# Kernel tuning notes

Measured on AMD Instinct MI355X. Metric: run time of the kernel, lower is better.

## Reference

```python
import jax, jax.numpy as jnp
import numpy as np

N_NODES = 50000
N_EDGES = 625000
D = 128          # hidden_dim
H = 8            # num_heads
DH = D // H      # head_dim
L = 4            # num_layers
F_IN = 64        # in_channels
G = 64           # num graphs
BETA = 1.0
EPS = 1e-5       # layernorm eps


def _seg_softmax(s, idx, n):
    # softmax of s over segments defined by idx (segments present in idx are never empty)
    m = jax.ops.segment_max(s, idx, num_segments=n)
    e = jnp.exp(s - m[idx])
    d = jax.ops.segment_sum(e, idx, num_segments=n)
    return e / d[idx]


def _ln(x, s, b):
    mu = jnp.mean(x, axis=-1, keepdims=True)
    var = jnp.var(x, axis=-1, keepdims=True)
    return (x - mu) / jnp.sqrt(var + EPS) * s + b


def _forward(x, edge_index, batch, node_W, node_b, cW1, cb1, cW2, cb2,
             qW, qb, kW, kb, vW, vb, oW, ob, bW, bb,
             f1W, f1b, f2W, f2b, n1s, n1b, n2s, n2b,
             outW1, outb1, outW2, outb2):
    N = x.shape[0]
    src, tgt = edge_index[0], edge_index[1]
    h = x @ node_W + node_b                              # [N, D]
    for l in range(L):
        # ---- dynamic curvature (attention-approximated Wasserstein) ----
        h_src, h_tgt = h[src], h[tgt]                    # [E, D]
        sim = jnp.sum(h_src * h_tgt, axis=-1) * BETA     # [E]
        alpha = _seg_softmax(sim, tgt, N)                # segment softmax over tgt
        dist = jnp.linalg.norm(h_src - h_tgt, axis=-1)   # [E]
        agg = jax.ops.segment_sum(alpha * dist, tgt, num_segments=N)
        curv = 1.0 - agg[tgt] / jnp.maximum(dist, 1e-6)  # [E]
        ce = jax.nn.relu(curv[:, None] @ cW1 + cb1) @ cW2 + cb2  # [E, D]
        # ---- CurvphormerLayer ----
        xn = _ln(h, n1s[l], n1b[l])
        q = (xn @ qW[l] + qb[l]).reshape(N, H, DH)
        k = (xn @ kW[l] + kb[l]).reshape(N, H, DH)
        v = (xn @ vW[l] + vb[l]).reshape(N, H, DH)
        scores = jnp.sum(q[src] * k[tgt], axis=-1) / (DH ** 0.5)  # [E, H]
        scores = scores + ce @ bW[l] + bb[l]                       # curvature bias
        probs = _seg_softmax(scores, tgt, N)                       # [E, H]
        msgs = (probs[..., None] * v[tgt]).reshape(-1, D)          # [E, D]
        aggm = jax.ops.segment_sum(msgs, src, num_segments=N)     # scatter to src
        h = h + (aggm @ oW[l] + ob[l])
        xn2 = _ln(h, n2s[l], n2b[l])
        h = h + (jax.nn.relu(xn2 @ f1W[l] + f1b[l]) @ f2W[l] + f2b[l])
    # ---- mean pool per graph ----
    counts = jnp.maximum(jax.ops.segment_sum(jnp.ones((N,), h.dtype), batch, num_segments=G), 1.0)
    g = jax.ops.segment_sum(h, batch, num_segments=G) / counts[:, None]
    return jax.nn.relu(g @ outW1 + outb1) @ outW2 + outb2


def setup_inputs() -> dict:
    keys = iter(jax.random.split(jax.random.key(0), 32))
    p = lambda shape, s=0.02: jax.random.normal(next(keys), shape, jnp.float32) * s
    x = jax.random.normal(next(keys), (N_NODES, F_IN), jnp.float32)
    edge_index = jax.random.randint(next(keys), (2, N_EDGES), 0, N_NODES)
    batch = jnp.sort(jax.random.randint(next(keys), (N_NODES,), 0, G))
    inp = {
        "x": x, "edge_index": edge_index, "batch": batch,
        "node_W": p((F_IN, D)), "node_b": p((D,)),
        "cW1": p((1, D)), "cb1": p((D,)), "cW2": p((D, D)), "cb2": p((D,)),
        "qW": p((L, D, D)), "qb": p((L, D)),
        "kW": p((L, D, D)), "kb": p((L, D)),
        "vW": p((L, D, D)), "vb": p((L, D)),
        "oW": p((L, D, D)), "ob": p((L, D)),
        "bW": p((L, D, H)), "bb": p((L, H)),
        "f1W": p((L, D, 4 * D)), "f1b": p((L, 4 * D)),
        "f2W": p((L, 4 * D, D)), "f2b": p((L, D)),
        "n1s": jnp.ones((L, D), jnp.float32), "n1b": jnp.zeros((L, D), jnp.float32),
        "n2s": jnp.ones((L, D), jnp.float32), "n2b": jnp.zeros((L, D), jnp.float32),
        "outW1": p((D, D // 2)), "outb1": p((D // 2,)),
        "outW2": p((D // 2, 1)), "outb2": p((1,)),
    }
    return inp


def reference(x, edge_index, batch, node_W, node_b, cW1, cb1, cW2, cb2,
              qW, qb, kW, kb, vW, vb, oW, ob, bW, bb,
              f1W, f1b, f2W, f2b, n1s, n1b, n2s, n2b,
              outW1, outb1, outW2, outb2):
    return _forward(x, edge_index, batch, node_W, node_b, cW1, cb1, cW2, cb2,
                    qW, qb, kW, kb, vW, vb, oW, ob, bW, bb,
                    f1W, f1b, f2W, f2b, n1s, n1b, n2s, n2b,
                    outW1, outb1, outW2, outb2)
```

## Files before the change

### kernel.cpp

```cpp
#include <hip/hip_runtime.h>

#define NN 50000
#define NE 625000
#define DD 128
#define HH 8
#define DHH 16
#define NL 4
#define FIN 64
#define NG 64
#define LN_EPS 1e-5f
#define NSEG 129
#define NT32 1563
#define NT64 782
#define NBS 196

typedef __bf16 bf16x8_t __attribute__((ext_vector_type(8)));
typedef unsigned short ushort8_t __attribute__((ext_vector_type(8)));
typedef float f32x4_t __attribute__((ext_vector_type(4)));
union BF8 { ushort8_t u; bf16x8_t b; };

__device__ __forceinline__ void fma4(float4& a, float s, float4 w) {
  a.x = fmaf(s, w.x, a.x); a.y = fmaf(s, w.y, a.y);
  a.z = fmaf(s, w.z, a.z); a.w = fmaf(s, w.w, a.w);
}
__device__ __forceinline__ unsigned short f2bf(float f) {
  unsigned u = __float_as_uint(f);
  unsigned r = ((u >> 16) & 1u) + 0x7FFFu;
  return (unsigned short)((u + r) >> 16);
}
__device__ __forceinline__ float bf2f(unsigned short u) {
  return __uint_as_float((unsigned)u << 16);
}

__device__ __forceinline__ void ln_tile_bf32(const float* __restrict__ h, int nb,
                                             const float* __restrict__ sc,
                                             const float* __restrict__ bi,
                                             ushort* xbf) {
  int tid = threadIdx.x;
  int r = tid >> 4, l16 = tid & 15;
  int nr = nb + r; if (nr >= NN) nr = NN - 1;
  const float* hp = h + (size_t)nr * DD + l16 * 8;
  float4 a0 = *(const float4*)hp;
  float4 a1 = *(const float4*)(hp + 4);
  float sum = a0.x + a0.y + a0.z + a0.w + a1.x + a1.y + a1.z + a1.w;
  float sq  = a0.x*a0.x + a0.y*a0.y + a0.z*a0.z + a0.w*a0.w
            + a1.x*a1.x + a1.y*a1.y + a1.z*a1.z + a1.w*a1.w;
#pragma unroll
  for (int off = 8; off >= 1; off >>= 1) {
    sum += __shfl_xor(sum, off, 64);
    sq  += __shfl_xor(sq,  off, 64);
  }
  float mu   = sum * (1.0f / DD);
  float var  = sq * (1.0f / DD) - mu * mu;
  float rstd = rsqrtf(var + LN_EPS);
  int d0 = l16 * 8;
  float4 s0 = *(const float4*)(sc + d0), s1 = *(const float4*)(sc + d0 + 4);
  float4 b0 = *(const float4*)(bi + d0), b1 = *(const float4*)(bi + d0 + 4);
  ushort8_t u;
  u[0] = f2bf((a0.x - mu) * rstd * s0.x + b0.x);
  u[1] = f2bf((a0.y - mu) * rstd * s0.y + b0.y);
  u[2] = f2bf((a0.z - mu) * rstd * s0.z + b0.z);
  u[3] = f2bf((a0.w - mu) * rstd * s0.w + b0.w);
  u[4] = f2bf((a1.x - mu) * rstd * s1.x + b1.x);
  u[5] = f2bf((a1.y - mu) * rstd * s1.y + b1.y);
  u[6] = f2bf((a1.z - mu) * rstd * s1.z + b1.z);
  u[7] = f2bf((a1.w - mu) * rstd * s1.w + b1.w);
  int off = (r * 256 + l16 * 16) ^ ((r & 7) << 4);
  *(ushort8_t*)((char*)xbf + off) = u;
}

__device__ __forceinline__ void ln_tile_bf64(const float* __restrict__ h, int nb,
                                             const float* __restrict__ sc,
                                             const float* __restrict__ bi,
                                             ushort* xbf) {
  int tid = threadIdx.x;
  int l16 = tid & 15;
  int d0 = l16 * 8;
  float4 s0 = *(const float4*)(sc + d0), s1 = *(const float4*)(sc + d0 + 4);
  float4 b0 = *(const float4*)(bi + d0), b1 = *(const float4*)(bi + d0 + 4);
#pragma unroll
  for (int p = 0; p < 2; p++) {
    int r = p * 32 + (tid >> 4);
    int nr = nb + r; if (nr >= NN) nr = NN - 1;
    const float* hp = h + (size_t)nr * DD + d0;
    float4 a0 = *(const float4*)hp;
    float4 a1 = *(const float4*)(hp + 4);
    float sum = a0.x + a0.y + a0.z + a0.w + a1.x + a1.y + a1.z + a1.w;
    float sq  = a0.x*a0.x + a0.y*a0.y + a0.z*a0.z + a0.w*a0.w
              + a1.x*a1.x + a1.y*a1.y + a1.z*a1.z + a1.w*a1.w;
#pragma unroll
    for (int off = 8; off >= 1; off >>= 1) {
      sum += __shfl_xor(sum, off, 64);
      sq  += __shfl_xor(sq,  off, 64);
    }
    float mu   = sum * (1.0f / DD);
    float var  = sq * (1.0f / DD) - mu * mu;
    float rstd = rsqrtf(var + LN_EPS);
    ushort8_t u;
    u[0] = f2bf((a0.x - mu) * rstd * s0.x + b0.x);
    u[1] = f2bf((a0.y - mu) * rstd * s0.y + b0.y);
    u[2] = f2bf((a0.z - mu) * rstd * s0.z + b0.z);
    u[3] = f2bf((a0.w - mu) * rstd * s0.w + b0.w);
    u[4] = f2bf((a1.x - mu) * rstd * s1.x + b1.x);
    u[5] = f2bf((a1.y - mu) * rstd * s1.y + b1.y);
    u[6] = f2bf((a1.z - mu) * rstd * s1.z + b1.z);
    u[7] = f2bf((a1.w - mu) * rstd * s1.w + b1.w);
    int off = (r * 256 + l16 * 16) ^ ((r & 7) << 4);
    *(ushort8_t*)((char*)xbf + off) = u;
  }
}

__global__ __launch_bounds__(256) void k_node_proj(const float* __restrict__ x,
                                                   const float* __restrict__ W,
                                                   const float* __restrict__ b,
                                                   float* __restrict__ h) {
  __shared__ float xt[8][FIN];
  int tid = threadIdx.x;
  int nb = blockIdx.x * 8;
  {
    int idx = tid * 2;
    *(float2*)&xt[idx >> 6][idx & 63] = *(const float2*)(x + (size_t)nb * FIN + idx);
  }
  __syncthreads();
  int c4 = (tid & 31) * 4;
  int r  = tid >> 5;
  float4 acc = *(const float4*)(b + c4);
  for (int k = 0; k < FIN; k += 4) {
    float4 xk = *(const float4*)&xt[r][k];
    const float* wp = W + (size_t)k * DD + c4;
    fma4(acc, xk.x, *(const float4*)wp);
    fma4(acc, xk.y, *(const float4*)(wp + DD));
    fma4(acc, xk.z, *(const float4*)(wp + 2 * DD));
    fma4(acc, xk.w, *(const float4*)(wp + 3 * DD));
  }
  *(float4*)(h + (size_t)(nb + r) * DD + c4) = acc;
}

__global__ __launch_bounds__(256) void k_edge1(const int* __restrict__ src_s, const int* __restrict__ tgt_s,
                                               const float* __restrict__ h, float* __restrict__ sim,
                                               float* __restrict__ dist) {
  int gid = blockIdx.x * 256 + threadIdx.x;
  int e = gid >> 4;
  if (e >= NE) return;
  int j = gid & 15;
  int s = src_s[e], t = tgt_s[e];
  const float4* ap = (const float4*)(h + (size_t)s * DD + j * 8);
  const float4* bp = (const float4*)(h + (size_t)t * DD + j * 8);
  float4 a0 = ap[0], a1 = ap[1];
  float4 b0 = bp[0], b1 = bp[1];
  float dot = 0.f, sq = 0.f;
  dot = fmaf(a0.x, b0.x, dot); dot = fmaf(a0.y, b0.y, dot);
  dot = fmaf(a0.z, b0.z, dot); dot = fmaf(a0.w, b0.w, dot);
  dot = fmaf(a1.x, b1.x, dot); dot = fmaf(a1.y, b1.y, dot);
  dot = fmaf(a1.z, b1.z, dot); dot = fmaf(a1.w, b1.w, dot);
  float d0 = a0.x - b0.x, d1 = a0.y - b0.y, d2 = a0.z - b0.z, d3 = a0.w - b0.w;
  float d4 = a1.x - b1.x, d5 = a1.y - b1.y, d6 = a1.z - b1.z, d7 = a1.w - b1.w;
  sq = fmaf(d0, d0, sq); sq = fmaf(d1, d1, sq); sq = fmaf(d2, d2, sq); sq = fmaf(d3, d3, sq);
  sq = fmaf(d4, d4, sq); sq = fmaf(d5, d5, sq); sq = fmaf(d6, d6, sq); sq = fmaf(d7, d7, sq);
#pragma unroll
  for (int off = 8; off >= 1; off >>= 1) {
    dot += __shfl_xor(dot, off, 64);
    sq  += __shfl_xor(sq,  off, 64);
  }
  if (j == 0) {
    sim[e]  = dot;
    dist[e] = sqrtf(sq);
  }
}

__global__ __launch_bounds__(256) void k_curva(const int* __restrict__ rowstart_t,
    const int* __restrict__ eid_t, const float* __restrict__ sim,
    const float* __restrict__ dist, float* __restrict__ aggv) {
  int node = blockIdx.x * 32 + (threadIdx.x >> 3);
  if (node >= NN) return;
  int j = threadIdx.x & 7;
  int rs = rowstart_t[node], re = rowstart_t[node + 1];
  float m = -3.4e38f;
  for (int i = rs + j; i < re; i += 8) m = fmaxf(m, sim[eid_t[i]]);
#pragma unroll
  for (int off = 1; off <= 4; off <<= 1) m = fmaxf(m, __shfl_xor(m, off, 64));
  float den = 0.f, nd = 0.f;
  for (int i = rs + j; i < re; i += 8) {
    int e = eid_t[i];
    float ev = expf(sim[e] - m);
    den += ev;
    nd = fmaf(ev, dist[e], nd);
  }
#pragma unroll
  for (int off = 1; off <= 4; off <<= 1) {
    den += __shfl_xor(den, off, 64);
    nd  += __shfl_xor(nd,  off, 64);
  }
  if (j == 0) aggv[node] = den > 0.f ? nd / den : 0.f;
}

__global__ __launch_bounds__(512) void k_ln_qkv(const float* __restrict__ h,
    const float* __restrict__ n1s_l, const float* __restrict__ n1b_l,
    const ushort* __restrict__ qkvT_l,
    const float* __restrict__ qb_l, const float* __restrict__ kb_l, const float* __restrict__ vb_l,
    ushort* __restrict__ q, ushort* __restrict__ kk, ushort* __restrict__ v) {
  __shared__ __align__(16) ushort xbf[32 * DD];
  int nb = blockIdx.x * 32;
  ln_tile_bf32(h, nb, n1s_l, n1b_l, xbf);
  __syncthreads();
  int lane = threadIdx.x & 63;
  int w = threadIdx.x >> 6;
  int g = lane >> 4, c = lane & 15;
  int xr = (c & 7) << 4;
  char* xb = (char*)xbf;
  BF8 a[2][4];
#pragma unroll
  for (int nt = 0; nt < 2; nt++)
#pragma unroll
    for (int kt = 0; kt < 4; kt++)
      a[nt][kt].u = *(ushort8_t*)(xb + (((nt * 16 + c) * 256 + kt * 64 + g * 16) ^ xr));
#pragma unroll
  for (int ti = 0; ti < 3; ti++) {
    int t = w * 3 + ti;
    int m = t >> 3;
    int colb = (t & 7) * 16;
    const float* bias = (m == 0 ? qb_l : (m == 1 ? kb_l : vb_l));
    float4 bv = *(const float4*)(bias + colb + g * 4);
    f32x4_t acc0 = {bv.x, bv.y, bv.z, bv.w};
    f32x4_t acc1 = acc0;
    const ushort* wp = qkvT_l + (size_t)(m * DD + colb + c) * DD + g * 8;
#pragma unroll
    for (int kt = 0; kt < 4; kt++) {
      BF8 b; b.u = *(const ushort8_t*)(wp + kt * 32);
      acc0 = __builtin_amdgcn_mfma_f32_16x16x32_bf16(b.b, a[0][kt].b, acc0, 0, 0, 0);
      acc1 = __builtin_amdgcn_mfma_f32_16x16x32_bf16(b.b, a[1][kt].b, acc1, 0, 0, 0);
    }
    ushort* out = (m == 0 ? q : (m == 1 ? kk : v));
    int n0 = nb + c;
    if (n0 < NN) {
      ushort4 o; o.x = f2bf(acc0[0]); o.y = f2bf(acc0[1]); o.z = f2bf(acc0[2]); o.w = f2bf(acc0[3]);
      *(ushort4*)(out + (size_t)n0 * DD + colb + g * 4) = o;
    }
    int n1 = nb + 16 + c;
    if (n1 < NN) {
      ushort4 o; o.x = f2bf(acc1[0]); o.y = f2bf(acc1[1]); o.z = f2bf(acc1[2]); o.w = f2bf(acc1[3]);
      *(ushort4*)(out + (size_t)n1 * DD + colb + g * 4) = o;
    }
  }
}

__global__ __launch_bounds__(256) void k_scores(const int* __restrict__ src_s, const int* __restrict__ tgt_s,
    const ushort* __restrict__ q, const ushort* __restrict__ k,
    const float* __restrict__ dist, const float* __restrict__ aggv,
    const float* __restrict__ bp_g,
    const float* __restrict__ slope_l, const float* __restrict__ inter_l,
    float* __restrict__ escore) {
  __shared__ float lsl[NSEG * HH], lin[NSEG * HH], bp[DD];
  __shared__ float lcurv[32];
  __shared__ int   lseg[32];
  int tid = threadIdx.x;
  for (int idx = tid; idx < NSEG * HH; idx += 256) { lsl[idx] = slope_l[idx]; lin[idx] = inter_l[idx]; }
  if (tid < DD) bp[tid] = bp_g[tid];
  __syncthreads();
  int eb = blockIdx.x * 32;
  if (tid < 32) {
    int e = eb + tid;
    if (e < NE) {
      int t = tgt_s[e];
      float curv = 1.0f - aggv[t] / fmaxf(dist[e], 1e-6f);
      int lo = 0, hi = DD;
      while (lo < hi) { int mid = (lo + hi) >> 1; if (bp[mid] < curv) lo = mid + 1; else hi = mid; }
      lcurv[tid] = curv;
      lseg[tid] = lo;
    }
  }
  __syncthreads();
  int gi = blockIdx.x * 256 + tid;
  if (gi >= NE * HH) return;
  int i = gi >> 3, hh = gi & 7;
  int s = src_s[i], t = tgt_s[i];
  int li = tid >> 3;
  float curv = lcurv[li];
  int seg = lseg[li];
  float bias = fmaf(lsl[seg * HH + hh], curv, lin[seg * HH + hh]);
  const ushort8_t* qp = (const ushort8_t*)(q + (size_t)s * DD + hh * DHH);
  const ushort8_t* kp = (const ushort8_t*)(k + (size_t)t * DD + hh * DHH);
  float dot = 0.f;
#pragma unroll
  for (int ii = 0; ii < 2; ii++) {
    ushort8_t a = qp[ii], b = kp[ii];
#pragma unroll
    for (int jj = 0; jj < 8; jj++) dot = fmaf(bf2f(a[jj]), bf2f(b[jj]), dot);
  }
  escore[gi] = dot * 0.25f + bias;
  (void)t;
}

__global__ __launch_bounds__(256) void k_softmax_t(const int* __restrict__ rowstart_t,
    const int* __restrict__ eid_t, float* __restrict__ escore, float* __restrict__ sdinv) {
  int node = blockIdx.x * 32 + (threadIdx.x >> 3);
  if (node >= NN) return;
  int hh = threadIdx.x & 7;
  int rs = rowstart_t[node], re = rowstart_t[node + 1];
  float m = -3.4e38f;
  int i = rs;
  for (; i + 4 <= re; i += 4) {
    int e0 = eid_t[i], e1 = eid_t[i + 1], e2 = eid_t[i + 2], e3 = eid_t[i + 3];
    float s0 = escore[e0 * HH + hh];
    float s1 = escore[e1 * HH + hh];
    float s2 = escore[e2 * HH + hh];
    float s3 = escore[e3 * HH + hh];
    m = fmaxf(m, s0); m = fmaxf(m, s1); m = fmaxf(m, s2); m = fmaxf(m, s3);
  }
  for (; i < re; i++) m = fmaxf(m, escore[eid_t[i] * HH + hh]);
  float sum = 0.f;
  i = rs;
  for (; i + 4 <= re; i += 4) {
    int e0 = eid_t[i], e1 = eid_t[i + 1], e2 = eid_t[i + 2], e3 = eid_t[i + 3];
    float p0 = expf(escore[e0 * HH + hh] - m);
    float p1 = expf(escore[e1 * HH + hh] - m);
    float p2 = expf(escore[e2 * HH + hh] - m);
    float p3 = expf(escore[e3 * HH + hh] - m);
    escore[e0 * HH + hh] = p0; escore[e1 * HH + hh] = p1;
    escore[e2 * HH + hh] = p2; escore[e3 * HH + hh] = p3;
    sum += p0; sum += p1; sum += p2; sum += p3;
  }
  for (; i < re; i++) {
    int e = eid_t[i];
    float p = expf(escore[e * HH + hh] - m);
    escore[e * HH + hh] = p;
    sum += p;
  }
  sdinv[node * HH + hh] = sum > 0.f ? 1.0f / sum : 0.f;
}

__global__ __launch_bounds__(256) void k_agg(const int* __restrict__ tgt_s,
    const int* __restrict__ rowstart,
    const float* __restrict__ escore, const float* __restrict__ sdinv,
    const ushort* __restrict__ v, ushort* __restrict__ aggmb) {
  int wave = (blockIdx.x * 256 + threadIdx.x) >> 6;
  int lane = threadIdx.x & 63;
  int rs = rowstart[wave], re = rowstart[wave + 1];
  int hh = lane >> 3;
  int d = lane * 2;
  float a0 = 0.f, a1 = 0.f;
  int i = rs;
  for (; i + 4 <= re; i += 4) {
    int t0 = tgt_s[i], t1 = tgt_s[i + 1], t2 = tgt_s[i + 2], t3 = tgt_s[i + 3];
    float e0 = escore[(i    ) * HH + hh];
    float e1 = escore[(i + 1) * HH + hh];
    float e2 = escore[(i + 2) * HH + hh];
    float e3 = escore[(i + 3) * HH + hh];
    float s0 = sdinv[t0 * HH + hh], s1 = sdinv[t1 * HH + hh];
    float s2 = sdinv[t2 * HH + hh], s3 = sdinv[t3 * HH + hh];
    ushort2 v0 = *(const ushort2*)(v + (size_t)t0 * DD + d);
    ushort2 v1 = *(const ushort2*)(v + (size_t)t1 * DD + d);
    ushort2 v2 = *(const ushort2*)(v + (size_t)t2 * DD + d);
    ushort2 v3 = *(const ushort2*)(v + (size_t)t3 * DD + d);
    float p0 = e0 * s0, p1 = e1 * s1, p2 = e2 * s2, p3 = e3 * s3;
    a0 = fmaf(p0, bf2f(v0.x), a0); a1 = fmaf(p0, bf2f(v0.y), a1);
    a0 = fmaf(p1, bf2f(v1.x), a0); a1 = fmaf(p1, bf2f(v1.y), a1);
    a0 = fmaf(p2, bf2f(v2.x), a0); a1 = fmaf(p2, bf2f(v2.y), a1);
    a0 = fmaf(p3, bf2f(v3.x), a0); a1 = fmaf(p3, bf2f(v3.y), a1);
  }
  for (; i < re; i++) {
    int t = tgt_s[i];
    float prob = escore[i * HH + hh] * sdinv[t * HH + hh];
    ushort2 vv = *(const ushort2*)(v + (size_t)t * DD + d);
    a0 = fmaf(prob, bf2f(vv.x), a0);
    a1 = fmaf(prob, bf2f(vv.y), a1);
  }
  ushort2 o; o.x = f2bf(a0); o.y = f2bf(a1);
  *(ushort2*)(aggmb + (size_t)wave * DD + d) = o;
}

__global__ __launch_bounds__(512) void k_update_o(const ushort* __restrict__ aggmb,
    const ushort* __restrict__ oT_l, const float* __restrict__ ob_l, float* __restrict__ h) {
  int nb = blockIdx.x * 32;
  int lane = threadIdx.x & 63, w = threadIdx.x >> 6;
  int g = lane >> 4, c = lane & 15;
  BF8 a[2][4];
#pragma unroll
  for (int nt = 0; nt < 2; nt++) {
    int na = nb + nt * 16 + c; if (na >= NN) na = NN - 1;
    const ushort* ap = aggmb + (size_t)na * DD + g * 8;
#pragma unroll
    for (int kt = 0; kt < 4; kt++) a[nt][kt].u = *(const ushort8_t*)(ap + kt * 32);
  }
  int colb = w * 16;
  float4 bv = *(const float4*)(ob_l + colb + g * 4);
  f32x4_t acc0 = {bv.x, bv.y, bv.z, bv.w};
  f32x4_t acc1 = acc0;
  const ushort* wp = oT_l + (size_t)(colb + c) * DD + g * 8;
#pragma unroll
  for (int kt = 0; kt < 4; kt++) {
    BF8 b; b.u = *(const ushort8_t*)(wp + kt * 32);
    acc0 = __builtin_amdgcn_mfma_f32_16x16x32_bf16(b.b, a[0][kt].b, acc0, 0, 0, 0);
    acc1 = __builtin_amdgcn_mfma_f32_16x16x32_bf16(b.b, a[1][kt].b, acc1, 0, 0, 0);
  }
#pragma unroll
  for (int nt = 0; nt < 2; nt++) {
    int node = nb + nt * 16 + c;
    if (node < NN) {
      float* hp = h + (size_t)node * DD + colb + g * 4;
      float4 hv = *(const float4*)hp;
      f32x4_t& acc = nt ? acc1 : acc0;
      hv.x += acc[0]; hv.y += acc[1]; hv.z += acc[2]; hv.w += acc[3];
      *(float4*)hp = hv;
    }
  }
}

__global__ __launch_bounds__(512) void k_ffn(const float* __restrict__ n2s_l, const float* __restrict__ n2b_l,
    const ushort* __restrict__ f1T_l, const float* __restrict__ f1b_l,
    const ushort* __restrict__ f2T_l, const float* __restrict__ f2b_l,
    float* __restrict__ h) {
  __shared__ __align__(16) ushort xbf[64 * DD];
  __shared__ __align__(16) ushort tbf[64 * 256];
  int nb = blockIdx.x * 64;
  ln_tile_bf64(h, nb, n2s_l, n2b_l, xbf);
  __syncthreads();
  int lane = threadIdx.x & 63, w = threadIdx.x >> 6;
  int g = lane >> 4, c = lane & 15;
  int xr = (c & 7) << 4;
  char* xb = (char*)xbf;
  char* tb = (char*)tbf;
  BF8 a[4][4];
#pragma unroll
  for (int nt = 0; nt < 4; nt++)
#pragma unroll
    for (int kt = 0; kt < 4; kt++)
      a[nt][kt].u = *(ushort8_t*)(xb + (((nt * 16 + c) * 256 + kt * 64 + g * 16) ^ xr));
  int colb2 = w * 16;
  float4 bv2 = *(const float4*)(f2b_l + colb2 + g * 4);
  f32x4_t o0 = {bv2.x, bv2.y, bv2.z, bv2.w};
  f32x4_t o1 = o0, o2 = o0, o3 = o0;
#pragma unroll
  for (int ch = 0; ch < 2; ch++) {
    if (ch) __syncthreads();
#pragma unroll
    for (int ti = 0; ti < 2; ti++) {
      int ctile = w * 2 + ti;
      int col = ch * 256 + ctile * 16;
      float4 bv = *(const float4*)(f1b_l + col + g * 4);
      f32x4_t ac0 = {bv.x, bv.y, bv.z, bv.w};
      f32x4_t ac1 = ac0, ac2 = ac0, ac3 = ac0;
      const ushort* wp = f1T_l + (size_t)(col + c) * DD + g * 8;
#pragma unroll
      for (int kt = 0; kt < 4; kt++) {
        BF8 b; b.u = *(const ushort8_t*)(wp + kt * 32);
        ac0 = __builtin_amdgcn_mfma_f32_16x16x32_bf16(b.b, a[0][kt].b, ac0, 0, 0, 0);
        ac1 = __builtin_amdgcn_mfma_f32_16x16x32_bf16(b.b, a[1][kt].b, ac1, 0, 0, 0);
        ac2 = __builtin_amdgcn_mfma_f32_16x16x32_bf16(b.b, a[2][kt].b, ac2, 0, 0, 0);
        ac3 = __builtin_amdgcn_mfma_f32_16x16x32_bf16(b.b, a[3][kt].b, ac3, 0, 0, 0);
      }
      int colL = (ctile * 16 + g * 4) * 2;
      {
        int row = c;
        ushort4 o4; o4.x = f2bf(fmaxf(ac0[0], 0.f)); o4.y = f2bf(fmaxf(ac0[1], 0.f));
        o4.z = f2bf(fmaxf(ac0[2], 0.f)); o4.w = f2bf(fmaxf(ac0[3], 0.f));
        *(ushort4*)(tb + ((row * 512 + colL) ^ ((row & 7) << 4))) = o4;
      }
      {
        int row = 16 + c;
        ushort4 o4; o4.x = f2bf(fmaxf(ac1[0], 0.f)); o4.y = f2bf(fmaxf(ac1[1], 0.f));
        o4.z = f2bf(fmaxf(ac1[2], 0.f)); o4.w = f2bf(fmaxf(ac1[3], 0.f));
        *(ushort4*)(tb + ((row * 512 + colL) ^ ((row & 7) << 4))) = o4;
      }
      {
        int row = 32 + c;
        ushort4 o4; o4.x = f2bf(fmaxf(ac2[0], 0.f)); o4.y = f2bf(fmaxf(ac2[1], 0.f));
        o4.z = f2bf(fmaxf(ac2[2], 0.f)); o4.w = f2bf(fmaxf(ac2[3], 0.f));
        *(ushort4*)(tb + ((row * 512 + colL) ^ ((row & 7) << 4))) = o4;
      }
      {
        int row = 48 + c;
        ushort4 o4; o4.x = f2bf(fmaxf(ac3[0], 0.f)); o4.y = f2bf(fmaxf(ac3[1], 0.f));
        o4.z = f2bf(fmaxf(ac3[2], 0.f)); o4.w = f2bf(fmaxf(ac3[3], 0.f));
        *(ushort4*)(tb + ((row * 512 + colL) ^ ((row & 7) << 4))) = o4;
      }
    }
    __syncthreads();
    const ushort* wp2 = f2T_l + (size_t)(colb2 + c) * 512 + ch * 256 + g * 8;
#pragma unroll
    for (int kt = 0; kt < 8; kt++) {
      BF8 b; b.u = *(const ushort8_t*)(wp2 + kt * 32);
      BF8 t0; t0.u = *(ushort8_t*)(tb + (((c) * 512 + kt * 64 + g * 16) ^ xr));
      BF8 t1; t1.u = *(ushort8_t*)(tb + (((16 + c) * 512 + kt * 64 + g * 16) ^ xr));
      BF8 t2; t2.u = *(ushort8_t*)(tb + (((32 + c) * 512 + kt * 64 + g * 16) ^ xr));
      BF8 t3; t3.u = *(ushort8_t*)(tb + (((48 + c) * 512 + kt * 64 + g * 16) ^ xr));
      o0 = __builtin_amdgcn_mfma_f32_16x16x32_bf16(b.b, t0.b, o0, 0, 0, 0);
      o1 = __builtin_amdgcn_mfma_f32_16x16x32_bf16(b.b, t1.b, o1, 0, 0, 0);
      o2 = __builtin_amdgcn_mfma_f32_16x16x32_bf16(b.b, t2.b, o2, 0, 0, 0);
      o3 = __builtin_amdgcn_mfma_f32_16x16x32_bf16(b.b, t3.b, o3, 0, 0, 0);
    }
  }
  {
    int node = nb + c;
    if (node < NN) {
      float* hp = h + (size_t)node * DD + colb2 + g * 4;
      float4 hv = *(const float4*)hp;
      hv.x += o0[0]; hv.y += o0[1]; hv.z += o0[2]; hv.w += o0[3];
      *(float4*)hp = hv;
    }
  }
  {
    int node = nb + 16 + c;
    if (node < NN) {
      float* hp = h + (size_t)node * DD + colb2 + g * 4;
      float4 hv = *(const float4*)hp;
      hv.x += o1[0]; hv.y += o1[1]; hv.z += o1[2]; hv.w += o1[3];
      *(float4*)hp = hv;
    }
  }
  {
    int node = nb + 32 + c;
    if (node < NN) {
      float* hp = h + (size_t)node * DD + colb2 + g * 4;
      float4 hv = *(const float4*)hp;
      hv.x += o2[0]; hv.y += o2[1]; hv.z += o2[2]; hv.w += o2[3];
      *(float4*)hp = hv;
    }
  }
  {
    int node = nb + 48 + c;
    if (node < NN) {
      float* hp = h + (size_t)node * DD + colb2 + g * 4;
      float4 hv = *(const float4*)hp;
      hv.x += o3[0]; hv.y += o3[1]; hv.z += o3[2]; hv.w += o3[3];
      *(float4*)hp = hv;
    }
  }
}

template <int K, int C>
__global__ void k_wt(const float* __restrict__ W, ushort* __restrict__ WT, int nm, int dstride) {
  int idx = blockIdx.x * 256 + threadIdx.x;
  if (idx >= K * C * nm) return;
  int mi = idx / (K * C), rem = idx - mi * (K * C);
  int cc = rem / K, kk2 = rem - cc * K;
  WT[(size_t)mi * dstride + cc * K + kk2] = f2bf(W[(size_t)mi * K * C + (size_t)kk2 * C + cc]);
}

__global__ void k_hist(const int* __restrict__ idxs, int* __restrict__ cnt) {
  int e = blockIdx.x * 256 + threadIdx.x;
  if (e < NE) atomicAdd(cnt + idxs[e], 1);
}

__global__ __launch_bounds__(256) void k_scan_blk(const int* __restrict__ cnt, int* __restrict__ bsum) {
  __shared__ int red[256];
  int tid = threadIdx.x;
  int idx = blockIdx.x * 256 + tid;
  red[tid] = (idx < NN) ? cnt[idx] : 0;
  __syncthreads();
  for (int off = 128; off >= 1; off >>= 1) {
    if (tid < off) red[tid] += red[tid + off];
    __syncthreads();
  }
  if (tid == 0) bsum[blockIdx.x] = red[0];
}

__global__ __launch_bounds__(256) void k_scan_top(const int* __restrict__ bsum,
                                                  int* __restrict__ boff, int* __restrict__ rowstart) {
  __shared__ int ps[256];
  int t = threadIdx.x;
  int v = (t < NBS) ? bsum[t] : 0;
  ps[t] = v;
  __syncthreads();
  for (int off = 1; off < 256; off <<= 1) {
    int x = (t >= off) ? ps[t - off] : 0;
    __syncthreads();
    ps[t] += x;
    __syncthreads();
  }
  boff[t] = ps[t] - v;
  if (t == 255) rowstart[NN] = ps[255];
}

__global__ __launch_bounds__(256) void k_scan_fin(const int* __restrict__ cnt,
                                                  const int* __restrict__ boff, int* __restrict__ rowstart) {
  __shared__ int ps[256];
  int t = threadIdx.x;
  int idx = blockIdx.x * 256 + t;
  int v = (idx < NN) ? cnt[idx] : 0;
  ps[t] = v;
  __syncthreads();
  for (int off = 1; off < 256; off <<= 1) {
    int x = (t >= off) ? ps[t - off] : 0;
    __syncthreads();
    ps[t] += x;
    __syncthreads();
  }
  if (idx < NN) rowstart[idx] = boff[blockIdx.x] + ps[t] - v;
}

__global__ void k_fill(const int* __restrict__ src, const int* __restrict__ tgt,
                       const int* __restrict__ rowstart,
                       int* __restrict__ cur, int* __restrict__ src_s, int* __restrict__ tgt_s) {
  int e = blockIdx.x * 256 + threadIdx.x;
  if (e >= NE) return;
  int s = src[e];
  int p = atomicAdd(cur + s, 1);
  int pos = rowstart[s] + p;
  src_s[pos] = s;
  tgt_s[pos] = tgt[e];
}

__global__ void k_fill_t(const int* __restrict__ tgt_s, const int* __restrict__ rowstart_t,
                         int* __restrict__ cur_t, int* __restrict__ eid_t) {
  int i = blockIdx.x * 256 + threadIdx.x;
  if (i >= NE) return;
  int t = tgt_s[i];
  int p = atomicAdd(cur_t + t, 1);
  eid_t[rowstart_t[t] + p] = i;
}

__global__ __launch_bounds__(64) void k_mbias_par(const float* __restrict__ cW2, const float* __restrict__ cb2,
                                                  const float* __restrict__ bW, const float* __restrict__ bb,
                                                  float* __restrict__ M, float* __restrict__ base) {
  int bid = blockIdx.x;
  int l = bid >> 7, d = bid & 127;
  int lane = threadIdx.x;
  int hh = lane >> 3, j0 = lane & 7;
  const float* bWl = bW + (size_t)l * DD * HH;
  float acc = 0.f;
#pragma unroll
  for (int t = 0; t < 16; t++) {
    int k = j0 + t * 8;
    acc = fmaf(cW2[d * DD + k], bWl[k * HH + hh], acc);
  }
#pragma unroll
  for (int off = 1; off <= 4; off <<= 1) acc += __shfl_xor(acc, off, 64);
  if (j0 == 0) M[(size_t)l * DD * HH + d * HH + hh] = acc;
  if (d == 0) {
    float bacc = 0.f;
#pragma unroll
    for (int t = 0; t < 16; t++) {
      int k = j0 + t * 8;
      bacc = fmaf(cb2[k], bWl[k * HH + hh], bacc);
    }
#pragma unroll
    for (int off = 1; off <= 4; off <<= 1) bacc += __shfl_xor(bacc, off, 64);
    if (j0 == 0) base[l * HH + hh] = bacc + bb[l * HH + hh];
  }
}

__global__ __launch_bounds__(128) void k_bp(const float* __restrict__ cW1, const float* __restrict__ cb1,
                                            float* __restrict__ bpg, int* __restrict__ posg) {
  __shared__ float x[DD], bp[DD];
  int tid = threadIdx.x;
  float c1v = cW1[tid], cbv = cb1[tid];
  x[tid] = (c1v == 0.f) ? __builtin_inff() : (-cbv / c1v);
  __syncthreads();
  float xv = x[tid]; int p = 0;
  for (int j = 0; j < DD; j++) {
    float xj = x[j];
    if (xj < xv || (xj == xv && j < tid)) p++;
  }
  bp[p] = xv;
  posg[tid] = p;
  __syncthreads();
  bpg[tid] = bp[tid];
}

__global__ __launch_bounds__(64) void k_pwl_tab(const float* __restrict__ cW1, const float* __restrict__ cb1,
    const int* __restrict__ posg, const float* __restrict__ Mb, const float* __restrict__ basel,
    float* __restrict__ slopeg, float* __restrict__ interg) {
  int bid = blockIdx.x;
  int l = bid / NSEG, s = bid - l * NSEG;
  int lane = threadIdx.x;
  int hh = lane >> 3, j0 = lane & 7;
  const float* M = Mb + (size_t)l * DD * HH;
  float sl = 0.f, in = 0.f;
#pragma unroll
  for (int t = 0; t < 16; t++) {
    int d = j0 + t * 8;
    float cv = cW1[d], cbv = cb1[d];
    int p = posg[d];
    bool act = (cv == 0.f) ? (cbv > 0.f) : ((cv > 0.f) ? (p < s) : (p >= s));
    float m = act ? M[d * HH + hh] : 0.f;
    sl = fmaf(cv, m, sl);
    in = fmaf(cbv, m, in);
  }
#pragma unroll
  for (int off = 1; off <= 4; off <<= 1) {
    sl += __shfl_xor(sl, off, 64);
    in += __shfl_xor(in, off, 64);
  }
  if (j0 == 0) {
    size_t o = (size_t)l * NSEG * HH + s * HH + hh;
    slopeg[o] = sl;
    interg[o] = in + basel[l * HH + hh];
  }
}

__global__ void k_bounds(const int* __restrict__ batch, int* __restrict__ gstart, int* __restrict__ gend) {
  int n = blockIdx.x * 256 + threadIdx.x;
  if (n >= NN) return;
  int b = batch[n];
  if (n == 0 || batch[n - 1] != b) gstart[b] = n;
  if (n == NN - 1 || batch[n + 1] != b) gend[b] = n + 1;
}

__global__ __launch_bounds__(256) void k_pool_part(const float* __restrict__ h,
    const int* __restrict__ batch, float* __restrict__ gpool) {
  int tid = threadIdx.x;
  int d = tid & 127, sub = tid >> 7;
  int n0 = blockIdx.x * 256;
  int nend = n0 + 256; if (nend > NN) nend = NN;
  float run = 0.f; int gcur = -1;
  for (int n = n0 + sub; n < nend; n += 2) {
    int g = batch[n];
    if (g != gcur) {
      if (gcur >= 0) atomicAdd(gpool + (size_t)gcur * DD + d, run);
      run = 0.f; gcur = g;
    }
    run += h[(size_t)n * DD + d];
  }
  if (gcur >= 0) atomicAdd(gpool + (size_t)gcur * DD + d, run);
}

__global__ __launch_bounds__(256) void k_head(const float* __restrict__ gpool,
    const int* __restrict__ gstart, const int* __restrict__ gend,
    const float* __restrict__ W1, const float* __restrict__ b1,
    const float* __restrict__ W2, const float* __restrict__ b2, float* __restrict__ out) {
  __shared__ float mid[NG * 64];
  int tid = threadIdx.x;
  for (int idx = tid; idx < NG * 64; idx += 256) {
    int g = idx >> 6, j = idx & 63;
    int cnt = gend[g] - gstart[g]; if (cnt < 1) cnt = 1;
    float rc = 1.0f / (float)cnt;
    float acc = 0.f;
    for (int d = 0; d < DD; d++) acc = fmaf(gpool[g * DD + d], W1[d * 64 + j], acc);
    mid[idx] = fmaxf(fmaf(acc, rc, b1[j]), 0.f);
  }
  __syncthreads();
  if (tid < NG) {
    float acc = b2[0];
    for (int j = 0; j < 64; j++) acc = fmaf(mid[tid * 64 + j], W2[j], acc);
    out[tid] = acc;
  }
}

extern "C" void kernel_launch(void* const* d_in, const int* in_sizes, int n_in,
                              void* d_out, int out_size, void* d_ws, size_t ws_size,
                              hipStream_t stream) {
  const float* x      = (const float*)d_in[0];
  const int*   ei     = (const int*)d_in[1];
  const int*   batch  = (const int*)d_in[2];
  const float* node_W = (const float*)d_in[3];
  const float* node_b = (const float*)d_in[4];
  const float* cW1    = (const float*)d_in[5];
  const float* cb1    = (const float*)d_in[6];
  const float* cW2    = (const float*)d_in[7];
  const float* cb2    = (const float*)d_in[8];
  const float* qW     = (const float*)d_in[9];
  const float* qb     = (const float*)d_in[10];
  const float* kW     = (const float*)d_in[11];
  const float* kb     = (const float*)d_in[12];
  const float* vW     = (const float*)d_in[13];
  const float* vb     = (const float*)d_in[14];
  const float* oW     = (const float*)d_in[15];
  const float* ob     = (const float*)d_in[16];
  const float* bW     = (const float*)d_in[17];
  const float* bb     = (const float*)d_in[18];
  const float* f1W    = (const float*)d_in[19];
  const float* f1b    = (const float*)d_in[20];
  const float* f2W    = (const float*)d_in[21];
  const float* f2b    = (const float*)d_in[22];
  const float* n1s    = (const float*)d_in[23];
  const float* n1b    = (const float*)d_in[24];
  const float* n2s    = (const float*)d_in[25];
  const float* n2b    = (const float*)d_in[26];
  const float* outW1  = (const float*)d_in[27];
  const float* outb1  = (const float*)d_in[28];
  const float* outW2  = (const float*)d_in[29];
  const float* outb2  = (const float*)d_in[30];

  const int* src = ei;
  const int* tgt = ei + NE;

  char* wp = (char*)d_ws;
  auto alloc = [&](size_t bytes) { void* p = (void*)wp; wp += (bytes + 255) & ~(size_t)255; return p; };
  float*    h       = (float*)alloc((size_t)NN * DD * 4);
  ushort*   q       = (ushort*)alloc((size_t)NN * DD * 2);
  ushort*   kk      = (ushort*)alloc((size_t)NN * DD * 2);
  ushort*   v       = (ushort*)alloc((size_t)NN * DD * 2);
  ushort*   aggmb   = (ushort*)alloc((size_t)NN * DD * 2);
  float*    sim     = (float*)alloc((size_t)NE * 4);
  float*    dist    = (float*)alloc((size_t)NE * 4);
  float*    escore  = (float*)alloc((size_t)NE * HH * 4);
  float*    sdinv   = (float*)alloc((size_t)NN * HH * 4);
  float*    aggv    = (float*)alloc((size_t)NN * 4);
  float*    Mb      = (float*)alloc((size_t)NL * DD * HH * 4);
  float*    basel   = (float*)alloc((size_t)NL * HH * 4);
  float*    bpg     = (float*)alloc((size_t)DD * 4);
  int*      posg    = (int*)alloc((size_t)DD * 4);
  float*    slopeg  = (float*)alloc((size_t)NL * NSEG * HH * 4);
  float*    interg  = (float*)alloc((size_t)NL * NSEG * HH * 4);
  int*      rowstart= (int*)alloc((size_t)(NN + 1) * 4);
  int*      rowstart_t = (int*)alloc((size_t)(NN + 1) * 4);
  int*      eid_t   = (int*)alloc((size_t)NE * 4);
  int*      src_s   = (int*)alloc((size_t)NE * 4);
  int*      tgt_s   = (int*)alloc((size_t)NE * 4);
  int*      cnt     = (int*)alloc((size_t)NN * 4);
  int*      cur     = (int*)alloc((size_t)NN * 4);
  int*      cnt_t   = (int*)alloc((size_t)NN * 4);
  int*      cur_t   = (int*)alloc((size_t)NN * 4);
  int*      bsum    = (int*)alloc((size_t)NBS * 4);
  int*      boff    = (int*)alloc((size_t)256 * 4);
  int*      gstart  = (int*)alloc((size_t)NG * 4);
  int*      gend    = (int*)alloc((size_t)NG * 4);
  float*    gpool   = (float*)alloc((size_t)NG * DD * 4);
  ushort*   qkvT    = (ushort*)alloc((size_t)NL * 3 * DD * DD * 2);
  ushort*   oT      = (ushort*)alloc((size_t)NL * DD * DD * 2);
  ushort*   f1T     = (ushort*)alloc((size_t)NL * DD * 512 * 2);
  ushort*   f2T     = (ushort*)alloc((size_t)NL * 512 * DD * 2);
  (void)in_sizes; (void)n_in; (void)out_size; (void)ws_size;

  hipMemsetAsync(cnt, 0, NN * 4, stream);
  hipMemsetAsync(cur, 0, NN * 4, stream);
  hipMemsetAsync(cnt_t, 0, NN * 4, stream);
  hipMemsetAsync(cur_t, 0, NN * 4, stream);
  hipMemsetAsync(gstart, 0, NG * 4, stream);
  hipMemsetAsync(gend, 0, NG * 4, stream);
  hipMemsetAsync(gpool, 0, NG * DD * 4, stream);
  k_hist<<<(NE + 255) / 256, 256, 0, stream>>>(src, cnt);
  k_scan_blk<<<NBS, 256, 0, stream>>>(cnt, bsum);
  k_scan_top<<<1, 256, 0, stream>>>(bsum, boff, rowstart);
  k_scan_fin<<<NBS, 256, 0, stream>>>(cnt, boff, rowstart);
  k_fill<<<(NE + 255) / 256, 256, 0, stream>>>(src, tgt, rowstart, cur, src_s, tgt_s);
  k_hist<<<(NE + 255) / 256, 256, 0, stream>>>(tgt, cnt_t);
  k_scan_blk<<<NBS, 256, 0, stream>>>(cnt_t, bsum);
  k_scan_top<<<1, 256, 0, stream>>>(bsum, boff, rowstart_t);
  k_scan_fin<<<NBS, 256, 0, stream>>>(cnt_t, boff, rowstart_t);
  k_fill_t<<<(NE + 255) / 256, 256, 0, stream>>>(tgt_s, rowstart_t, cur_t, eid_t);
  k_mbias_par<<<NL * DD, 64, 0, stream>>>(cW2, cb2, bW, bb, Mb, basel);
  k_bp<<<1, 128, 0, stream>>>(cW1, cb1, bpg, posg);
  k_pwl_tab<<<NL * NSEG, 64, 0, stream>>>(cW1, cb1, posg, Mb, basel, slopeg, interg);
  k_bounds<<<(NN + 255) / 256, 256, 0, stream>>>(batch, gstart, gend);
  k_wt<DD, DD><<<(NL * DD * DD + 255) / 256, 256, 0, stream>>>(qW, qkvT,               NL, 3 * DD * DD);
  k_wt<DD, DD><<<(NL * DD * DD + 255) / 256, 256, 0, stream>>>(kW, qkvT + DD * DD,     NL, 3 * DD * DD);
  k_wt<DD, DD><<<(NL * DD * DD + 255) / 256, 256, 0, stream>>>(vW, qkvT + 2 * DD * DD, NL, 3 * DD * DD);
  k_wt<DD, DD><<<(NL * DD * DD + 255) / 256, 256, 0, stream>>>(oW, oT, NL, DD * DD);
  k_wt<DD, 512><<<(NL * DD * 512 + 255) / 256, 256, 0, stream>>>(f1W, f1T, NL, DD * 512);
  k_wt<512, DD><<<(NL * DD * 512 + 255) / 256, 256, 0, stream>>>(f2W, f2T, NL, DD * 512);
  k_node_proj<<<NN / 8, 256, 0, stream>>>(x, node_W, node_b, h);

  for (int l = 0; l < NL; l++) {
    k_edge1<<<(NE * 16 + 255) / 256, 256, 0, stream>>>(src_s, tgt_s, h, sim, dist);
    k_curva<<<NT32, 256, 0, stream>>>(rowstart_t, eid_t, sim, dist, aggv);
    k_ln_qkv<<<NT32, 512, 0, stream>>>(h, n1s + l * DD, n1b + l * DD,
        qkvT + (size_t)l * 3 * DD * DD,
        qb + l * DD, kb + l * DD, vb + l * DD, q, kk, v);
    k_scores<<<(NE * HH + 255) / 256, 256, 0, stream>>>(src_s, tgt_s, q, kk,
        dist, aggv, bpg,
        slopeg + (size_t)l * NSEG * HH, interg + (size_t)l * NSEG * HH,
        escore);
    k_softmax_t<<<NT32, 256, 0, stream>>>(rowstart_t, eid_t, escore, sdinv);
    k_agg<<<NN / 4, 256, 0, stream>>>(tgt_s, rowstart, escore, sdinv, v, aggmb);
    k_update_o<<<NT32, 512, 0, stream>>>(aggmb, oT + (size_t)l * DD * DD, ob + l * DD, h);
    k_ffn<<<NT64, 512, 0, stream>>>(n2s + l * DD, n2b + l * DD,
        f1T + (size_t)l * DD * 512, f1b + (size_t)l * 4 * DD,
        f2T + (size_t)l * 512 * DD, f2b + l * DD, h);
  }
  k_pool_part<<<(NN + 255) / 256, 256, 0, stream>>>(h, batch, gpool);
  k_head<<<1, 256, 0, stream>>>(gpool, gstart, gend, outW1, outb1, outW2, outb2, (float*)d_out);
}
```

Before: 1.450 ms.

## Stop writing back softmax exps; recompute in aggregation from stored max/sum

The segment softmax kernel no longer scatters exp values back into the edge score buffer. It stores the per-node-per-head max and inverse sum instead, and the aggregation kernel recomputes exp(score - max) * invsum on the fly. This removes a random scatter-write of the E*H score array, at the cost of extra exp work and 8-byte gathers in k_agg. Separately, the node projection kernel now stages the weight matrix in shared memory and computes 4 rows per thread over 32-node blocks.

```diff
diff --git a/kernel.cpp b/kernel.cpp
--- a/kernel.cpp
+++ b/kernel.cpp
@@ -114,26 +114,34 @@
                                                    const float* __restrict__ W,
                                                    const float* __restrict__ b,
                                                    float* __restrict__ h) {
-  __shared__ float xt[8][FIN];
+  __shared__ float Wl[FIN * DD];
+  __shared__ float xt[32][FIN];
   int tid = threadIdx.x;
-  int nb = blockIdx.x * 8;
-  {
-    int idx = tid * 2;
-    *(float2*)&xt[idx >> 6][idx & 63] = *(const float2*)(x + (size_t)nb * FIN + idx);
+  int nb = blockIdx.x * 32;
+  for (int i = tid * 4; i < FIN * DD; i += 1024)
+    *(float4*)&Wl[i] = *(const float4*)(W + i);
+  for (int i = tid * 4; i < 32 * FIN; i += 1024) {
+    int row = i >> 6, cc = i & 63;
+    int node = nb + row; if (node >= NN) node = NN - 1;
+    *(float4*)&xt[row][cc] = *(const float4*)(x + (size_t)node * FIN + cc);
   }
   __syncthreads();
   int c4 = (tid & 31) * 4;
-  int r  = tid >> 5;
-  float4 acc = *(const float4*)(b + c4);
-  for (int k = 0; k < FIN; k += 4) {
-    float4 xk = *(const float4*)&xt[r][k];
-    const float* wp = W + (size_t)k * DD + c4;
-    fma4(acc, xk.x, *(const float4*)wp);
-    fma4(acc, xk.y, *(const float4*)(wp + DD));
-    fma4(acc, xk.z, *(const float4*)(wp + 2 * DD));
-    fma4(acc, xk.w, *(const float4*)(wp + 3 * DD));
-  }
-  *(float4*)(h + (size_t)(nb + r) * DD + c4) = acc;
+  int r0 = (tid >> 5) * 4;
+  float4 bv = *(const float4*)(b + c4);
+  float4 a0 = bv, a1 = bv, a2 = bv, a3 = bv;
+  for (int k = 0; k < FIN; k++) {
+    float4 wv = *(const float4*)&Wl[k * DD + c4];
+    fma4(a0, xt[r0][k], wv);
+    fma4(a1, xt[r0 + 1][k], wv);
+    fma4(a2, xt[r0 + 2][k], wv);
+    fma4(a3, xt[r0 + 3][k], wv);
+  }
+  int n0 = nb + r0;
+  if (n0 < NN)     *(float4*)(h + (size_t)n0 * DD + c4) = a0;
+  if (n0 + 1 < NN) *(float4*)(h + (size_t)(n0 + 1) * DD + c4) = a1;
+  if (n0 + 2 < NN) *(float4*)(h + (size_t)(n0 + 2) * DD + c4) = a2;
+  if (n0 + 3 < NN) *(float4*)(h + (size_t)(n0 + 3) * DD + c4) = a3;
 }
 
 __global__ __launch_bounds__(256) void k_edge1(const int* __restrict__ src_s, const int* __restrict__ tgt_s,
@@ -292,7 +300,7 @@
 }
 
 __global__ __launch_bounds__(256) void k_softmax_t(const int* __restrict__ rowstart_t,
-    const int* __restrict__ eid_t, float* __restrict__ escore, float* __restrict__ sdinv) {
+    const int* __restrict__ eid_t, const float* __restrict__ escore, float2* __restrict__ msd) {
   int node = blockIdx.x * 32 + (threadIdx.x >> 3);
   if (node >= NN) return;
   int hh = threadIdx.x & 7;
@@ -316,22 +324,16 @@
     float p1 = expf(escore[e1 * HH + hh] - m);
     float p2 = expf(escore[e2 * HH + hh] - m);
     float p3 = expf(escore[e3 * HH + hh] - m);
-    escore[e0 * HH + hh] = p0; escore[e1 * HH + hh] = p1;
-    escore[e2 * HH + hh] = p2; escore[e3 * HH + hh] = p3;
     sum += p0; sum += p1; sum += p2; sum += p3;
   }
-  for (; i < re; i++) {
-    int e = eid_t[i];
-    float p = expf(escore[e * HH + hh] - m);
-    escore[e * HH + hh] = p;
-    sum += p;
-  }
-  sdinv[node * HH + hh] = sum > 0.f ? 1.0f / sum : 0.f;
+  for (; i < re; i++) sum += expf(escore[eid_t[i] * HH + hh] - m);
+  float2 o; o.x = m; o.y = sum > 0.f ? 1.0f / sum : 0.f;
+  msd[(size_t)node * HH + hh] = o;
 }
 
 __global__ __launch_bounds__(256) void k_agg(const int* __restrict__ tgt_s,
     const int* __restrict__ rowstart,
-    const float* __restrict__ escore, const float* __restrict__ sdinv,
+    const float* __restrict__ escore, const float2* __restrict__ msd,
     const ushort* __restrict__ v, ushort* __restrict__ aggmb) {
   int wave = (blockIdx.x * 256 + threadIdx.x) >> 6;
   int lane = threadIdx.x & 63;
@@ -346,13 +348,16 @@
     float e1 = escore[(i + 1) * HH + hh];
     float e2 = escore[(i + 2) * HH + hh];
     float e3 = escore[(i + 3) * HH + hh];
-    float s0 = sdinv[t0 * HH + hh], s1 = sdinv[t1 * HH + hh];
-    float s2 = sdinv[t2 * HH + hh], s3 = sdinv[t3 * HH + hh];
+    float2 m0 = msd[(size_t)t0 * HH + hh], m1 = msd[(size_t)t1 * HH + hh];
+    float2 m2 = msd[(size_t)t2 * HH + hh], m3 = msd[(size_t)t3 * HH + hh];
     ushort2 v0 = *(const ushort2*)(v + (size_t)t0 * DD + d);
     ushort2 v1 = *(const ushort2*)(v + (size_t)t1 * DD + d);
     ushort2 v2 = *(const ushort2*)(v + (size_t)t2 * DD + d);
     ushort2 v3 = *(const ushort2*)(v + (size_t)t3 * DD + d);
-    float p0 = e0 * s0, p1 = e1 * s1, p2 = e2 * s2, p3 = e3 * s3;
+    float p0 = expf(e0 - m0.x) * m0.y;
+    float p1 = expf(e1 - m1.x) * m1.y;
+    float p2 = expf(e2 - m2.x) * m2.y;
+    float p3 = expf(e3 - m3.x) * m3.y;
     a0 = fmaf(p0, bf2f(v0.x), a0); a1 = fmaf(p0, bf2f(v0.y), a1);
     a0 = fmaf(p1, bf2f(v1.x), a0); a1 = fmaf(p1, bf2f(v1.y), a1);
     a0 = fmaf(p2, bf2f(v2.x), a0); a1 = fmaf(p2, bf2f(v2.y), a1);
@@ -360,7 +365,8 @@
   }
   for (; i < re; i++) {
     int t = tgt_s[i];
-    float prob = escore[i * HH + hh] * sdinv[t * HH + hh];
+    float2 md = msd[(size_t)t * HH + hh];
+    float prob = expf(escore[i * HH + hh] - md.x) * md.y;
     ushort2 vv = *(const ushort2*)(v + (size_t)t * DD + d);
     a0 = fmaf(prob, bf2f(vv.x), a0);
     a1 = fmaf(prob, bf2f(vv.y), a1);
@@ -785,7 +791,7 @@
   float*    sim     = (float*)alloc((size_t)NE * 4);
   float*    dist    = (float*)alloc((size_t)NE * 4);
   float*    escore  = (float*)alloc((size_t)NE * HH * 4);
-  float*    sdinv   = (float*)alloc((size_t)NN * HH * 4);
+  float2*   msd     = (float2*)alloc((size_t)NN * HH * 8);
   float*    aggv    = (float*)alloc((size_t)NN * 4);
   float*    Mb      = (float*)alloc((size_t)NL * DD * HH * 4);
   float*    basel   = (float*)alloc((size_t)NL * HH * 4);
@@ -840,7 +846,7 @@
   k_wt<DD, DD><<<(NL * DD * DD + 255) / 256, 256, 0, stream>>>(oW, oT, NL, DD * DD);
   k_wt<DD, 512><<<(NL * DD * 512 + 255) / 256, 256, 0, stream>>>(f1W, f1T, NL, DD * 512);
   k_wt<512, DD><<<(NL * DD * 512 + 255) / 256, 256, 0, stream>>>(f2W, f2T, NL, DD * 512);
-  k_node_proj<<<NN / 8, 256, 0, stream>>>(x, node_W, node_b, h);
+  k_node_proj<<<NT32, 256, 0, stream>>>(x, node_W, node_b, h);
 
   for (int l = 0; l < NL; l++) {
     k_edge1<<<(NE * 16 + 255) / 256, 256, 0, stream>>>(src_s, tgt_s, h, sim, dist);
@@ -852,8 +858,8 @@
         dist, aggv, bpg,
         slopeg + (size_t)l * NSEG * HH, interg + (size_t)l * NSEG * HH,
         escore);
-    k_softmax_t<<<NT32, 256, 0, stream>>>(rowstart_t, eid_t, escore, sdinv);
-    k_agg<<<NN / 4, 256, 0, stream>>>(tgt_s, rowstart, escore, sdinv, v, aggmb);
+    k_softmax_t<<<NT32, 256, 0, stream>>>(rowstart_t, eid_t, escore, msd);
+    k_agg<<<NN / 4, 256, 0, stream>>>(tgt_s, rowstart, escore, msd, v, aggmb);
     k_update_o<<<NT32, 512, 0, stream>>>(aggmb, oT + (size_t)l * DD * DD, ob + l * DD, h);
     k_ffn<<<NT64, 512, 0, stream>>>(n2s + l * DD, n2b + l * DD,
         f1T + (size_t)l * DD * 512, f1b + (size_t)l * 4 * DD,
```

Result: faster. 1.407 ms (-2.9%).
